# Performance work log

Hardware: AMD Instinct MI355X
Metric: run time of the kernel (lower is better)

Reference implementation:

```python
import jax, jax.numpy as jnp
import numpy as np

EPS = 1e-7


def ciou_pairwise(b1, b2):
    # b1: (N,1,4), b2: (1,N,4) in xyxy; returns (N,N) CIoU
    b1x1, b1y1, b1x2, b1y2 = b1[..., 0], b1[..., 1], b1[..., 2], b1[..., 3]
    b2x1, b2y1, b2x2, b2y2 = b2[..., 0], b2[..., 1], b2[..., 2], b2[..., 3]

    # intersection
    iw = jnp.clip(jnp.minimum(b1x2, b2x2) - jnp.maximum(b1x1, b2x1), 0.0)
    ih = jnp.clip(jnp.minimum(b1y2, b2y2) - jnp.maximum(b1y1, b2y1), 0.0)
    inter = iw * ih

    w1, h1 = b1x2 - b1x1, b1y2 - b1y1
    w2, h2 = b2x2 - b2x1, b2y2 - b2y1
    union = w1 * h1 + w2 * h2 - inter + EPS
    iou = inter / union

    # smallest enclosing box diagonal
    cw = jnp.maximum(b1x2, b2x2) - jnp.minimum(b1x1, b2x1)
    ch = jnp.maximum(b1y2, b2y2) - jnp.minimum(b1y1, b2y1)
    c2 = cw * cw + ch * ch + EPS

    # squared center distance
    rho2 = ((b2x1 + b2x2 - b1x1 - b1x2) ** 2 + (b2y1 + b2y2 - b1y1 - b1y2) ** 2) / 4.0

    # aspect-ratio consistency term
    v = (4.0 / (np.pi ** 2)) * (jnp.arctan(w2 / (h2 + EPS)) - jnp.arctan(w1 / (h1 + EPS))) ** 2
    alpha = jax.lax.stop_gradient(v / (v - iou + (1.0 + EPS)))
    return iou - (rho2 / c2 + v * alpha)


def setup_inputs() -> dict:
    key = jax.random.key(0)
    k1, k2, k3 = jax.random.split(key, 3)
    N = 4096
    conf = jax.random.uniform(k1, (N, 1), dtype=jnp.float32)           # confidence in [0,1)
    xy1 = jax.random.uniform(k2, (N, 2), dtype=jnp.float32) * 600.0    # top-left corner
    wh = jax.random.uniform(k3, (N, 2), dtype=jnp.float32) * 100.0 + 1.0  # width/height >= 1
    x = jnp.concatenate([conf, xy1, xy1 + wh], axis=1)                 # (N, 5): conf, x1, y1, x2, y2
    gamma = jnp.zeros((1,), dtype=jnp.float32)
    return {"x": x, "gamma": gamma}


def reference(x, gamma):
    boxes = x[:, 1:]
    conf = x[:, 0]
    iou = ciou_pairwise(boxes[:, None, :], boxes[None, :, :])          # (N, N)
    conf_matrix = conf[:, None] * conf[None, :]                        # (N, N) outer product
    attention = jax.nn.softmax(iou * conf_matrix, axis=-1)             # (N, N)
    x_prime = x * gamma + attention @ x                                # (N, 5)
    return jax.nn.sigmoid(x_prime)
```

## Files before the change

kernel.cpp:

```cpp
#include <hip/hip_runtime.h>
#include <math.h>

#define N 4096
#define FEPS 1e-7f
#define BLK 256
#define JT 64
#define CH (N / JT)
#define FSTRIDE 12
#define N6 (N * 6)

#define PART_OFF (N * FSTRIDE)

__global__ void precompute_kernel(const float* __restrict__ x, float* __restrict__ f) {
    int i = blockIdx.x * blockDim.x + threadIdx.x;
    if (i >= N) return;
    float cf = x[i * 5 + 0], x1 = x[i * 5 + 1], y1 = x[i * 5 + 2];
    float x2 = x[i * 5 + 3], y2 = x[i * 5 + 4];
    float w = x2 - x1, h = y2 - y1;
    float* fi = f + (size_t)i * FSTRIDE;
    fi[0] = cf; fi[1] = x1; fi[2] = y1; fi[3] = x2; fi[4] = y2;
    fi[5] = (x1 + x2) * 0.5f; fi[6] = (y1 + y2) * 0.5f; fi[7] = w; fi[8] = h;
    fi[9] = w * h + 0.5f * FEPS;
    fi[10] = 0.6366197723675814f * atanf(w / (h + FEPS));
    fi[11] = cf * 1.2011224087864498f;
}

__global__ __launch_bounds__(BLK) void ciou_attn_kernel(
        const float* __restrict__ f,
        float* __restrict__ part) {
    const int gb = blockIdx.x / JT;
    const int jt = blockIdx.x % JT;
    const int i = gb * BLK + threadIdx.x;

    const float4* fi = (const float4*)(f + (size_t)i * FSTRIDE);
    float4 A = fi[0], B = fi[1], C = fi[2];
    const float rx1 = A.y, ry1 = A.z, rx2 = A.w;
    const float ry2 = B.x, rhx = B.y, rhy = B.z, rw = B.w;
    const float rh = C.x, rareps = C.y, rat = C.z, rcf2 = C.w;

    float sum = 0.f, a0 = 0.f, a1 = 0.f, a2 = 0.f, a3 = 0.f, a4 = 0.f;
    const float ONEP = 1.f + FEPS;
    const float* fj = f + (size_t)(jt * CH) * FSTRIDE;

#pragma unroll 4
    for (int jj = 0; jj < CH; jj++, fj += FSTRIDE) {
        float jcf = fj[0], jx1 = fj[1], jy1 = fj[2], jx2 = fj[3], jy2 = fj[4];
        float jhx = fj[5], jhy = fj[6], jw = fj[7], jh = fj[8];
        float jareps = fj[9], jat = fj[10], jcf2 = fj[11];

        float iwr = fminf(rx2, jx2) - fmaxf(rx1, jx1);
        float ihr = fminf(ry2, jy2) - fmaxf(ry1, jy1);
        float iw = fmaxf(iwr, 0.f);
        float ih = fmaxf(ihr, 0.f);
        float inter = iw * ih;
        float uni = (rareps + jareps) - inter;
        float iou = fminf(inter * __builtin_amdgcn_rcpf(uni), 1.0f);
        float cw = (rw + jw) - iwr;
        float ch = (rh + jh) - ihr;
        float c2 = cw * cw + ch * ch + FEPS;
        float dx = jhx - rhx;
        float dy = jhy - rhy;
        float rho2 = dx * dx + dy * dy;
        float da = jat - rat;
        float v = da * da;
        float den = (v - iou) + ONEP;
        float valpha = v * v * __builtin_amdgcn_rcpf(den);
        float ciou = iou - (rho2 * __builtin_amdgcn_rcpf(c2) + valpha);
        float e = __builtin_amdgcn_exp2f(ciou * (rcf2 * jcf2));
        sum += e;
        a0 += e * jcf;
        a1 += e * jx1;
        a2 += e * jy1;
        a3 += e * jx2;
        a4 += e * jy2;
    }

    float* p = part + (size_t)jt * N6 + (size_t)i * 6;
    p[0] = sum; p[1] = a0; p[2] = a1; p[3] = a2; p[4] = a3; p[5] = a4;
}

__global__ void epilogue_kernel(const float* __restrict__ x,
                                const float* __restrict__ gamma,
                                const float* __restrict__ part,
                                float* __restrict__ out) {
    int idx = blockIdx.x * blockDim.x + threadIdx.x;
    if (idx >= N * 5) return;
    int i = idx / 5, c = idx % 5;
    float se = 0.f, a = 0.f;
    const float* p = part + (size_t)i * 6;
#pragma unroll 8
    for (int jt = 0; jt < JT; jt++) {
        se += p[jt * (size_t)N6 + 0];
        a  += p[jt * (size_t)N6 + 1 + c];
    }
    float xp = x[idx] * gamma[0] + a / se;
    out[idx] = 1.f / (1.f + expf(-xp));
}

extern "C" void kernel_launch(void* const* d_in, const int* in_sizes, int n_in,
                              void* d_out, int out_size, void* d_ws, size_t ws_size,
                              hipStream_t stream) {
    const float* x = (const float*)d_in[0];
    const float* gamma = (const float*)d_in[1];
    float* out = (float*)d_out;
    float* f = (float*)d_ws;
    float* part = (float*)d_ws + PART_OFF;

    precompute_kernel<<<(N + 255) / 256, 256, 0, stream>>>(x, f);
    ciou_attn_kernel<<<(N / BLK) * JT, BLK, 0, stream>>>(f, part);
    epilogue_kernel<<<(N * 5 + 255) / 256, 256, 0, stream>>>(x, gamma, part, out);
}
```

Before: 87.77 us.

## Fuse box precompute into attention kernel and stage j-tile in shared memory

Removes the separate precompute kernel. Each attention block now computes its own row record and its 64 j-box records (including atanf) directly from x, and stages the j-tile in LDS. The inner loop reads from shared memory instead of global/scalar loads, and explicit fmaf is used for several expressions. This saves one launch and a workspace round trip, but adds a __syncthreads and recomputes atanf redundantly in every block (1024 blocks each doing 256+64 records).

Measured after the change: 83.84 us. 4.5% less time.

```diff
diff --git a/kernel.cpp b/kernel.cpp
--- a/kernel.cpp
+++ b/kernel.cpp
@@ -6,44 +6,46 @@
 #define BLK 256
 #define JT 64
 #define CH (N / JT)
-#define FSTRIDE 12
+#define LSTRIDE 12
 #define N6 (N * 6)
 
-#define PART_OFF (N * FSTRIDE)
 
-__global__ void precompute_kernel(const float* __restrict__ x, float* __restrict__ f) {
-    int i = blockIdx.x * blockDim.x + threadIdx.x;
-    if (i >= N) return;
+__device__ __forceinline__ void box_record(const float* __restrict__ x, int i, float* rec) {
     float cf = x[i * 5 + 0], x1 = x[i * 5 + 1], y1 = x[i * 5 + 2];
     float x2 = x[i * 5 + 3], y2 = x[i * 5 + 4];
     float w = x2 - x1, h = y2 - y1;
-    float* fi = f + (size_t)i * FSTRIDE;
-    fi[0] = cf; fi[1] = x1; fi[2] = y1; fi[3] = x2; fi[4] = y2;
-    fi[5] = (x1 + x2) * 0.5f; fi[6] = (y1 + y2) * 0.5f; fi[7] = w; fi[8] = h;
-    fi[9] = w * h + 0.5f * FEPS;
-    fi[10] = 0.6366197723675814f * atanf(w / (h + FEPS));
-    fi[11] = cf * 1.2011224087864498f;
+    rec[0] = cf; rec[1] = x1; rec[2] = y1; rec[3] = x2; rec[4] = y2;
+    rec[5] = (x1 + x2) * 0.5f; rec[6] = (y1 + y2) * 0.5f; rec[7] = w; rec[8] = h;
+    rec[9] = w * h + 0.5f * FEPS;
+    rec[10] = 0.6366197723675814f * atanf(w / (h + FEPS));
+    rec[11] = cf * 1.2011224087864498f;
 }
 
 __global__ __launch_bounds__(BLK) void ciou_attn_kernel(
-        const float* __restrict__ f,
+        const float* __restrict__ x,
         float* __restrict__ part) {
+    __shared__ float jrec[CH * LSTRIDE];
+    const int tid = threadIdx.x;
     const int gb = blockIdx.x / JT;
     const int jt = blockIdx.x % JT;
-    const int i = gb * BLK + threadIdx.x;
+    const int i = gb * BLK + tid;
 
-    const float4* fi = (const float4*)(f + (size_t)i * FSTRIDE);
-    float4 A = fi[0], B = fi[1], C = fi[2];
-    const float rx1 = A.y, ry1 = A.z, rx2 = A.w;
-    const float ry2 = B.x, rhx = B.y, rhy = B.z, rw = B.w;
-    const float rh = C.x, rareps = C.y, rat = C.z, rcf2 = C.w;
+    if (tid < CH) box_record(x, jt * CH + tid, &jrec[tid * LSTRIDE]);
+
+    float R[12];
+    box_record(x, i, R);
+    const float rx1 = R[1], ry1 = R[2], rx2 = R[3], ry2 = R[4];
+    const float rhx = R[5], rhy = R[6], rw = R[7], rh = R[8];
+    const float rareps = R[9], rat = R[10], rcf2 = R[11];
+
+    __syncthreads();
 
     float sum = 0.f, a0 = 0.f, a1 = 0.f, a2 = 0.f, a3 = 0.f, a4 = 0.f;
     const float ONEP = 1.f + FEPS;
-    const float* fj = f + (size_t)(jt * CH) * FSTRIDE;
 
 #pragma unroll 4
-    for (int jj = 0; jj < CH; jj++, fj += FSTRIDE) {
+    for (int jj = 0; jj < CH; jj++) {
+        const float* fj = &jrec[jj * LSTRIDE];
         float jcf = fj[0], jx1 = fj[1], jy1 = fj[2], jx2 = fj[3], jy2 = fj[4];
         float jhx = fj[5], jhy = fj[6], jw = fj[7], jh = fj[8];
         float jareps = fj[9], jat = fj[10], jcf2 = fj[11];
@@ -57,22 +59,22 @@
         float iou = fminf(inter * __builtin_amdgcn_rcpf(uni), 1.0f);
         float cw = (rw + jw) - iwr;
         float ch = (rh + jh) - ihr;
-        float c2 = cw * cw + ch * ch + FEPS;
+        float c2 = fmaf(cw, cw, fmaf(ch, ch, FEPS));
         float dx = jhx - rhx;
         float dy = jhy - rhy;
-        float rho2 = dx * dx + dy * dy;
+        float rho2 = fmaf(dx, dx, dy * dy);
         float da = jat - rat;
         float v = da * da;
         float den = (v - iou) + ONEP;
-        float valpha = v * v * __builtin_amdgcn_rcpf(den);
-        float ciou = iou - (rho2 * __builtin_amdgcn_rcpf(c2) + valpha);
+        float valpha = (v * v) * __builtin_amdgcn_rcpf(den);
+        float ciou = iou - fmaf(rho2, __builtin_amdgcn_rcpf(c2), valpha);
         float e = __builtin_amdgcn_exp2f(ciou * (rcf2 * jcf2));
         sum += e;
-        a0 += e * jcf;
-        a1 += e * jx1;
-        a2 += e * jy1;
-        a3 += e * jx2;
-        a4 += e * jy2;
+        a0 = fmaf(e, jcf, a0);
+        a1 = fmaf(e, jx1, a1);
+        a2 = fmaf(e, jy1, a2);
+        a3 = fmaf(e, jx2, a3);
+        a4 = fmaf(e, jy2, a4);
     }
 
     float* p = part + (size_t)jt * N6 + (size_t)i * 6;
@@ -103,10 +105,8 @@
     const float* x = (const float*)d_in[0];
     const float* gamma = (const float*)d_in[1];
     float* out = (float*)d_out;
-    float* f = (float*)d_ws;
-    float* part = (float*)d_ws + PART_OFF;
+    float* part = (float*)d_ws;
 
-    precompute_kernel<<<(N + 255) / 256, 256, 0, stream>>>(x, f);
-    ciou_attn_kernel<<<(N / BLK) * JT, BLK, 0, stream>>>(f, part);
+    ciou_attn_kernel<<<(N / BLK) * JT, BLK, 0, stream>>>(x, part);
     epilogue_kernel<<<(N * 5 + 255) / 256, 256, 0, stream>>>(x, gamma, part, out);
 }
```
